# Performance work log

Measured on AMD Instinct MI355X. Metric: run time of the kernel, lower is better.

Reference implementation:

```python
import jax, jax.numpy as jnp
from jax import lax
import numpy as np

B, T, I, H, O = 2048, 512, 3, 128, 2


def _uniform(key, shape, scale):
    return jax.random.uniform(key, shape, jnp.float32, -scale, scale)


def setup_inputs() -> dict:
    key = jax.random.key(0)
    ks = jax.random.split(key, 12)
    s = 1.0 / np.sqrt(H)  # PyTorch LSTM init scale
    inp = {
        "x": jax.random.normal(ks[0], (B, T, I), jnp.float32),
        # layer 0: input size I
        "w_ih0": _uniform(ks[1], (4 * H, I), s),
        "w_hh0": _uniform(ks[2], (4 * H, H), s),
        "b_ih0": _uniform(ks[3], (4 * H,), s),
        "b_hh0": _uniform(ks[4], (4 * H,), s),
        # layer 1: input size H
        "w_ih1": _uniform(ks[5], (4 * H, H), s),
        "w_hh1": _uniform(ks[6], (4 * H, H), s),
        "b_ih1": _uniform(ks[7], (4 * H,), s),
        "b_hh1": _uniform(ks[8], (4 * H,), s),
        # final projection
        "fc_w": _uniform(ks[9], (O, H), 1.0 / np.sqrt(H)),
        "fc_b": _uniform(ks[10], (O,), 1.0 / np.sqrt(H)),
    }
    return inp


def _lstm_layer(x, w_ih, w_hh, b_ih, b_hh):
    # x: [B, T, D_in] -> hidden sequence [B, T, H]
    b, t, _ = x.shape
    h_dim = w_hh.shape[1]
    # precompute input projections for all timesteps (one big GEMM)
    x_proj = jnp.einsum("btd,gd->btg", x, w_ih) + b_ih + b_hh  # [B, T, 4H]
    x_proj = jnp.swapaxes(x_proj, 0, 1)  # [T, B, 4H]

    def step(carry, xt):
        h, c = carry
        gates = xt + h @ w_hh.T  # [B, 4H]
        i, f, g, o = jnp.split(gates, 4, axis=-1)  # PyTorch gate order i,f,g,o
        i = jax.nn.sigmoid(i)
        f = jax.nn.sigmoid(f)
        g = jnp.tanh(g)
        o = jax.nn.sigmoid(o)
        c = f * c + i * g
        h = o * jnp.tanh(c)
        return (h, c), h

    h0 = jnp.zeros((b, h_dim), x.dtype)
    c0 = jnp.zeros((b, h_dim), x.dtype)
    _, hs = lax.scan(step, (h0, c0), x_proj)  # hs: [T, B, H]
    return jnp.swapaxes(hs, 0, 1)  # [B, T, H]


def reference(x, w_ih0, w_hh0, b_ih0, b_hh0, w_ih1, w_hh1, b_ih1, b_hh1, fc_w, fc_b):
    h1 = _lstm_layer(x, w_ih0, w_hh0, b_ih0, b_hh0)   # [B, T, H]
    h2 = _lstm_layer(h1, w_ih1, w_hh1, b_ih1, b_hh1)  # [B, T, H]
    last = h2[:, -1, :]                                # [B, H]
    return last @ fc_w.T + fc_b                        # [B, O]
```

## Files before the change

kernel.cpp:

```cpp
#include <hip/hip_runtime.h>

#define B_   2048
#define T_   512
#define H_   128
#define G_   512
#define R_   8
#define NTHR 512

typedef _Float16 f16;
typedef _Float16 f16x8 __attribute__((ext_vector_type(8)));
typedef float    f32x4 __attribute__((ext_vector_type(4)));
typedef int      i32x2 __attribute__((ext_vector_type(2)));

#define OFF_W1    0
#define OFF_RING  131072
#define OFF_HB    139264
#define OFF_XT    143360
#define LDS_BYTES 145408

__device__ __forceinline__ float rcp_(float v) {
#if __has_builtin(__builtin_amdgcn_rcpf)
  return __builtin_amdgcn_rcpf(v);
#else
  return 1.0f / v;
#endif
}
__device__ __forceinline__ float sig_(float v)  { return rcp_(1.0f + __expf(-v)); }
__device__ __forceinline__ float tanh_(float v) { return 1.0f - 2.0f * rcp_(__expf(2.0f * v) + 1.0f); }

__device__ __forceinline__ f16x8 cvt8(const float* __restrict__ p) {
  float4 a = ((const float4*)p)[0];
  float4 b = ((const float4*)p)[1];
  f16x8 v;
  v[0]=(f16)a.x; v[1]=(f16)a.y; v[2]=(f16)a.z; v[3]=(f16)a.w;
  v[4]=(f16)b.x; v[5]=(f16)b.y; v[6]=(f16)b.z; v[7]=(f16)b.w;
  return v;
}
__device__ __forceinline__ f32x4 mfma16(f16x8 a, f16x8 b, f32x4 c) {
  return __builtin_amdgcn_mfma_f32_16x16x32_f16(a, b, c, 0, 0, 0);
}

__device__ __forceinline__ void pls2_(float a, float b, float& x, float& y) {
#if __has_builtin(__builtin_amdgcn_permlane32_swap)
  i32x2 r = __builtin_amdgcn_permlane32_swap(__float_as_int(a), __float_as_int(b),
                                             false, false);
  x = __int_as_float(r.x); y = __int_as_float(r.y);
#else
  asm volatile("v_permlane32_swap_b32 %0, %1" : "+v"(a), "+v"(b));
  x = a; y = b;
#endif
}

__global__ __launch_bounds__(NTHR, 2)
void lstm_v6(const float* __restrict__ x,
             const float* __restrict__ w_ih0, const float* __restrict__ w_hh0,
             const float* __restrict__ b_ih0, const float* __restrict__ b_hh0,
             const float* __restrict__ w_ih1, const float* __restrict__ w_hh1,
             const float* __restrict__ b_ih1, const float* __restrict__ b_hh1,
             const float* __restrict__ fc_w,  const float* __restrict__ fc_b,
             float* __restrict__ out)
{
  extern __shared__ char lds[];
  char*  w1L   = lds + OFF_W1;
  char*  ringB = lds + OFF_RING;
  char*  hBB   = lds + OFF_HB;
  char*  xT    = lds + OFF_XT;

  const int tid  = (int)threadIdx.x;
  const int lane = tid & 63;
  const int wv   = tid >> 6;
  const int n    = lane & 15;
  const int hi   = lane >> 4;
  const int u0   = wv * 16;
  const int blk  = (int)blockIdx.x;
  const int rsw  = (n & 7) << 4;

  for (int idx = tid; idx < G_*16; idx += NTHR) {
    const int g = idx >> 4, s7 = idx & 15;
    f16x8 v = cvt8(w_ih1 + g*H_ + s7*8);
    *(f16x8*)(w1L + g*256 + ((s7*16) ^ ((g&7)<<4))) = v;
  }
  for (int i = tid; i < 3584; i += NTHR) ((unsigned*)ringB)[i] = 0u;
  __syncthreads();

  float xr0 = 0.f, xr1 = 0.f, xr2 = 0.f;
  if (wv == 7) {
    const int tok = lane >> 3, r = lane & 7;
    const size_t base = (size_t)(blk*R_ + r) * T_;
    const float a0 = x[(base + tok)*3+0];
    const float a1 = x[(base + tok)*3+1];
    const float a2 = x[(base + tok)*3+2];
    f16* w = (f16*)(xT + tok*128 + r*16);
    w[0] = (f16)a0; w[1] = (f16)a1; w[2] = (f16)a2;
    xr0 = x[(base + 8 + tok)*3+0];
    xr1 = x[(base + 8 + tok)*3+1];
    xr2 = x[(base + 8 + tok)*3+2];
  }

  f16x8 whh0f[4][4], whh1f[4][4];
  #pragma unroll
  for (int q = 0; q < 4; ++q)
    #pragma unroll
    for (int kc = 0; kc < 4; ++kc) {
      const int off = (q*H_ + u0 + n)*H_ + kc*32 + hi*8;
      whh0f[q][kc] = cvt8(w_hh0 + off);
      whh1f[q][kc] = cvt8(w_hh1 + off);
    }
  f16x8 w0p[4];
  float b0[4], bP[4];
  #pragma unroll
  for (int q = 0; q < 4; ++q) {
    const int g = q*H_ + u0 + n;
    b0[q] = b_ih0[g] + b_hh0[g];
    bP[q] = b_ih1[g] + b_hh1[g];
    f16x8 z;
    #pragma unroll
    for (int e = 0; e < 8; ++e) z[e] = (f16)0.f;
    if (hi == 0) {
      z[0] = (f16)w_ih0[g*3+0];
      z[1] = (f16)w_ih0[g*3+1];
      z[2] = (f16)w_ih0[g*3+2];
    }
    w0p[q] = z;
  }

  int offA[4];
  #pragma unroll
  for (int kc = 0; kc < 4; ++kc)
    offA[kc] = (n&7)*256 + ((kc*64 + hi*16) ^ rsw);

  float cA0 = 0.f, cA1 = 0.f, cB0 = 0.f, cB1 = 0.f;
  f32x4 xpP[4];
  const int rowbase = (hi & 1)*4 + ((lane >= 32) ? 2 : 0);
  const int colb    = 2*(u0 + n);
  __syncthreads();

  for (int s = 0; s < T_ + 2; ++s) {
    if (wv == 7 && (s & 7) == 3) {
      const int c = s >> 3;
      const int tok = lane >> 3, r = lane & 7;
      if (c <= 61) {
        const size_t base = (size_t)(blk*R_ + r) * T_ + (8*(c+2) + tok);
        const float a0 = x[base*3+0], a1 = x[base*3+1], a2 = x[base*3+2];
        f16* w = (f16*)(xT + ((c+1)&1)*1024 + tok*128 + r*16);
        w[0] = (f16)xr0; w[1] = (f16)xr1; w[2] = (f16)xr2;
        xr0 = a0; xr1 = a1; xr2 = a2;
      } else if (c == 62) {
        f16* w = (f16*)(xT + ((c+1)&1)*1024 + tok*128 + r*16);
        w[0] = (f16)xr0; w[1] = (f16)xr1; w[2] = (f16)xr2;
      }
    }

    if ((s & 1) == 0 && s >= 2 && s <= T_) {
      const char* pa = ringB + ((n < 8) ? (((s-2)&3)*2048) : (((s-1)&3)*2048));
      #pragma unroll
      for (int q = 0; q < 4; ++q)
        { xpP[q][0]=bP[q]; xpP[q][1]=bP[q]; xpP[q][2]=bP[q]; xpP[q][3]=bP[q]; }
      #pragma unroll
      for (int kc = 0; kc < 4; ++kc) {
        const f16x8 a = *(const f16x8*)(pa + offA[kc]);
        #pragma unroll
        for (int q = 0; q < 4; ++q) {
          const f16x8 bf = *(const f16x8*)(w1L + (q*H_ + u0 + n)*256
                                           + ((kc*64 + hi*16) ^ rsw));
          xpP[q] = mfma16(a, bf, xpP[q]);
        }
      }
    }

    if (s < T_) {
      const f16x8 ax = *(const f16x8*)(xT + ((s>>3)&1)*1024 + (s&7)*128 + (n&7)*16);
      f32x4 acc[4];
      #pragma unroll
      for (int q = 0; q < 4; ++q) {
        f32x4 a; a[0]=b0[q]; a[1]=b0[q]; a[2]=b0[q]; a[3]=b0[q];
        acc[q] = mfma16(ax, w0p[q], a);
      }
      const char* pa = ringB + ((s-1)&3)*2048;
      #pragma unroll
      for (int kc = 0; kc < 4; ++kc) {
        const f16x8 af = *(const f16x8*)(pa + offA[kc]);
        #pragma unroll
        for (int q = 0; q < 4; ++q) acc[q] = mfma16(af, whh0f[q][kc], acc[q]);
      }
      char* wr = ringB + (s&3)*2048;
      float gA[4], gB[4], d0, d1;
      #pragma unroll
      for (int q = 0; q < 4; ++q) {
        pls2_(acc[q][0], acc[q][2], gA[q], d0);
        pls2_(acc[q][1], acc[q][3], gB[q], d1);
      }
      {
        const float iv = sig_(gA[0]), fv = sig_(gA[1]), gv = tanh_(gA[2]), ov = sig_(gA[3]);
        cA0 = fv*cA0 + iv*gv;
        const float h = ov * tanh_(cA0);
        *(f16*)(wr + rowbase*256 + (colb ^ (rowbase<<4))) = (f16)h;
      }
      {
        const float iv = sig_(gB[0]), fv = sig_(gB[1]), gv = tanh_(gB[2]), ov = sig_(gB[3]);
        cA1 = fv*cA1 + iv*gv;
        const float h = ov * tanh_(cA1);
        *(f16*)(wr + (rowbase+1)*256 + (colb ^ ((rowbase+1)<<4))) = (f16)h;
      }
    }

    if (s >= 2) {
      const bool odd = (s & 1);
      const char* pb = hBB + (s&1)*2048;
      f32x4 acc[4];
      #pragma unroll
      for (int q = 0; q < 4; ++q) acc[q] = xpP[q];
      #pragma unroll
      for (int kc = 0; kc < 4; ++kc) {
        const f16x8 af = *(const f16x8*)(pb + offA[kc]);
        #pragma unroll
        for (int q = 0; q < 4; ++q) acc[q] = mfma16(af, whh1f[q][kc], acc[q]);
      }
      char* wr = hBB + ((s+1)&1)*2048;
      float gA[4], gB[4];
      #pragma unroll
      for (int q = 0; q < 4; ++q) {
        float ex, ey, fx, fy;
        pls2_(acc[q][0], acc[q][2], ex, ey);
        gA[q] = odd ? ey : ex;
        pls2_(acc[q][1], acc[q][3], fx, fy);
        gB[q] = odd ? fy : fx;
      }
      {
        const float iv = sig_(gA[0]), fv = sig_(gA[1]), gv = tanh_(gA[2]), ov = sig_(gA[3]);
        cB0 = fv*cB0 + iv*gv;
        const float h = ov * tanh_(cB0);
        *(f16*)(wr + rowbase*256 + (colb ^ (rowbase<<4))) = (f16)h;
      }
      {
        const float iv = sig_(gB[0]), fv = sig_(gB[1]), gv = tanh_(gB[2]), ov = sig_(gB[3]);
        cB1 = fv*cB1 + iv*gv;
        const float h = ov * tanh_(cB1);
        *(f16*)(wr + (rowbase+1)*256 + (colb ^ ((rowbase+1)<<4))) = (f16)h;
      }
    }
    __syncthreads();
  }

  if (tid < R_*2) {
    const int r = tid >> 1, o = tid & 1;
    float acc = fc_b[o];
    #pragma unroll 4
    for (int d = 0; d < H_; ++d) {
      const f16 hv = *(const f16*)(hBB + r*256 + ((2*d) ^ ((r&7)<<4)));
      acc += (float)hv * fc_w[o*H_ + d];
    }
    out[(blk*R_ + r)*2 + o] = acc;
  }
}

extern "C" void kernel_launch(void* const* d_in, const int* in_sizes, int n_in,
                              void* d_out, int out_size, void* d_ws, size_t ws_size,
                              hipStream_t stream) {
  const float* x     = (const float*)d_in[0];
  const float* w_ih0 = (const float*)d_in[1];
  const float* w_hh0 = (const float*)d_in[2];
  const float* b_ih0 = (const float*)d_in[3];
  const float* b_hh0 = (const float*)d_in[4];
  const float* w_ih1 = (const float*)d_in[5];
  const float* w_hh1 = (const float*)d_in[6];
  const float* b_ih1 = (const float*)d_in[7];
  const float* b_hh1 = (const float*)d_in[8];
  const float* fc_w  = (const float*)d_in[9];
  const float* fc_b  = (const float*)d_in[10];
  (void)in_sizes; (void)n_in; (void)out_size; (void)d_ws; (void)ws_size;

  hipFuncSetAttribute((const void*)lstm_v6,
                      hipFuncAttributeMaxDynamicSharedMemorySize, LDS_BYTES);

  lstm_v6<<<B_/R_, NTHR, LDS_BYTES, stream>>>(
      x, w_ih0, w_hh0, b_ih0, b_hh0, w_ih1, w_hh1, b_ih1, b_hh1,
      fc_w, fc_b, (float*)d_out);
}
```

Before: 884.8 us.

## Batch layer-1 input projection over four timesteps and pack h stores in pairs

Enlarges the layer-0 hidden-state ring from 4 to 8 slots so the layer-1 input projection runs every fourth step over two timestep pairs, reusing each loaded W_ih1 fragment for two MFMAs. This halves the LDS weight reads for that projection. Separately, hidden-state writes are packed two f16 values per 32-bit store by exchanging with the neighbouring lane via DPP, so only even lanes write. The cost is a layer-1 pipeline two steps deeper, more LDS, and more accumulator registers, which may pressure the two-blocks-per-CU occupancy.

```diff
diff --git a/kernel.cpp b/kernel.cpp
--- a/kernel.cpp
+++ b/kernel.cpp
@@ -14,9 +14,9 @@
 
 #define OFF_W1    0
 #define OFF_RING  131072
-#define OFF_HB    139264
-#define OFF_XT    143360
-#define LDS_BYTES 145408
+#define OFF_HB    147456
+#define OFF_XT    151552
+#define LDS_BYTES 153600
 
 __device__ __forceinline__ float rcp_(float v) {
 #if __has_builtin(__builtin_amdgcn_rcpf)
@@ -51,8 +51,19 @@
 #endif
 }
 
+__device__ __forceinline__ unsigned packpair_(float h) {
+  const f16 hf = (f16)h;
+  unsigned u = (unsigned)__builtin_bit_cast(unsigned short, hf);
+#if __has_builtin(__builtin_amdgcn_mov_dpp)
+  unsigned p = (unsigned)__builtin_amdgcn_mov_dpp((int)u, 0xB1, 0xF, 0xF, true);
+#else
+  unsigned p = (unsigned)__shfl_xor((int)u, 1);
+#endif
+  return u | (p << 16);
+}
+
 __global__ __launch_bounds__(NTHR, 2)
-void lstm_v6(const float* __restrict__ x,
+void lstm_v8(const float* __restrict__ x,
              const float* __restrict__ w_ih0, const float* __restrict__ w_hh0,
              const float* __restrict__ b_ih0, const float* __restrict__ b_hh0,
              const float* __restrict__ w_ih1, const float* __restrict__ w_hh1,
@@ -80,7 +91,7 @@
     f16x8 v = cvt8(w_ih1 + g*H_ + s7*8);
     *(f16x8*)(w1L + g*256 + ((s7*16) ^ ((g&7)<<4))) = v;
   }
-  for (int i = tid; i < 3584; i += NTHR) ((unsigned*)ringB)[i] = 0u;
+  for (int i = tid; i < 5632; i += NTHR) ((unsigned*)ringB)[i] = 0u;
   __syncthreads();
 
   float xr0 = 0.f, xr1 = 0.f, xr2 = 0.f;
@@ -128,14 +139,19 @@
   #pragma unroll
   for (int kc = 0; kc < 4; ++kc)
     offA[kc] = (n&7)*256 + ((kc*64 + hi*16) ^ rsw);
+  int offB[4];
+  #pragma unroll
+  for (int kc = 0; kc < 4; ++kc)
+    offB[kc] = (kc*64 + hi*16) ^ rsw;
 
   float cA0 = 0.f, cA1 = 0.f, cB0 = 0.f, cB1 = 0.f;
-  f32x4 xpP[4];
+  f32x4 xpA[4], xpB[4];
   const int rowbase = (hi & 1)*4 + ((lane >= 32) ? 2 : 0);
-  const int colb    = 2*(u0 + n);
+  const int colb    = 2*(u0 + (n & ~1));
+  const bool wlane  = ((n & 1) == 0);
   __syncthreads();
 
-  for (int s = 0; s < T_ + 2; ++s) {
+  for (int s = 0; s < T_ + 4; ++s) {
     if (wv == 7 && (s & 7) == 3) {
       const int c = s >> 3;
       const int tok = lane >> 3, r = lane & 7;
@@ -151,19 +167,23 @@
       }
     }
 
-    if ((s & 1) == 0 && s >= 2 && s <= T_) {
-      const char* pa = ringB + ((n < 8) ? (((s-2)&3)*2048) : (((s-1)&3)*2048));
-      #pragma unroll
-      for (int q = 0; q < 4; ++q)
-        { xpP[q][0]=bP[q]; xpP[q][1]=bP[q]; xpP[q][2]=bP[q]; xpP[q][3]=bP[q]; }
+    if ((s & 3) == 0 && s >= 4 && s <= T_) {
+      const char* pa0 = ringB + ((n < 8) ? (((s-4)&7)*2048) : (((s-3)&7)*2048));
+      const char* pa1 = ringB + ((n < 8) ? (((s-2)&7)*2048) : (((s-1)&7)*2048));
+      #pragma unroll
+      for (int q = 0; q < 4; ++q) {
+        xpA[q][0]=bP[q]; xpA[q][1]=bP[q]; xpA[q][2]=bP[q]; xpA[q][3]=bP[q];
+        xpB[q][0]=bP[q]; xpB[q][1]=bP[q]; xpB[q][2]=bP[q]; xpB[q][3]=bP[q];
+      }
       #pragma unroll
       for (int kc = 0; kc < 4; ++kc) {
-        const f16x8 a = *(const f16x8*)(pa + offA[kc]);
+        const f16x8 a0 = *(const f16x8*)(pa0 + offA[kc]);
+        const f16x8 a1 = *(const f16x8*)(pa1 + offA[kc]);
         #pragma unroll
         for (int q = 0; q < 4; ++q) {
-          const f16x8 bf = *(const f16x8*)(w1L + (q*H_ + u0 + n)*256
-                                           + ((kc*64 + hi*16) ^ rsw));
-          xpP[q] = mfma16(a, bf, xpP[q]);
+          const f16x8 bf = *(const f16x8*)(w1L + (q*H_ + u0 + n)*256 + offB[kc]);
+          xpA[q] = mfma16(a0, bf, xpA[q]);
+          xpB[q] = mfma16(a1, bf, xpB[q]);
         }
       }
     }
@@ -176,14 +196,14 @@
         f32x4 a; a[0]=b0[q]; a[1]=b0[q]; a[2]=b0[q]; a[3]=b0[q];
         acc[q] = mfma16(ax, w0p[q], a);
       }
-      const char* pa = ringB + ((s-1)&3)*2048;
+      const char* pa = ringB + (((s-1)&7)*2048);
       #pragma unroll
       for (int kc = 0; kc < 4; ++kc) {
         const f16x8 af = *(const f16x8*)(pa + offA[kc]);
         #pragma unroll
         for (int q = 0; q < 4; ++q) acc[q] = mfma16(af, whh0f[q][kc], acc[q]);
       }
-      char* wr = ringB + (s&3)*2048;
+      char* wr = ringB + ((s&7)*2048);
       float gA[4], gB[4], d0, d1;
       #pragma unroll
       for (int q = 0; q < 4; ++q) {
@@ -193,50 +213,60 @@
       {
         const float iv = sig_(gA[0]), fv = sig_(gA[1]), gv = tanh_(gA[2]), ov = sig_(gA[3]);
         cA0 = fv*cA0 + iv*gv;
-        const float h = ov * tanh_(cA0);
-        *(f16*)(wr + rowbase*256 + (colb ^ (rowbase<<4))) = (f16)h;
+        const unsigned pk = packpair_(ov * tanh_(cA0));
+        if (wlane)
+          *(unsigned*)(wr + rowbase*256 + (colb ^ (rowbase<<4))) = pk;
       }
       {
         const float iv = sig_(gB[0]), fv = sig_(gB[1]), gv = tanh_(gB[2]), ov = sig_(gB[3]);
         cA1 = fv*cA1 + iv*gv;
-        const float h = ov * tanh_(cA1);
-        *(f16*)(wr + (rowbase+1)*256 + (colb ^ ((rowbase+1)<<4))) = (f16)h;
-      }
-    }
-
-    if (s >= 2) {
-      const bool odd = (s & 1);
+        const unsigned pk = packpair_(ov * tanh_(cA1));
+        if (wlane)
+          *(unsigned*)(wr + (rowbase+1)*256 + (colb ^ ((rowbase+1)<<4))) = pk;
+      }
+    }
+
+    if (s >= 4) {
+      const int  p   = s & 3;
+      const bool odd = (p & 1) != 0;
       const char* pb = hBB + (s&1)*2048;
       f32x4 acc[4];
-      #pragma unroll
-      for (int q = 0; q < 4; ++q) acc[q] = xpP[q];
+      if (p < 2) {
+        #pragma unroll
+        for (int q = 0; q < 4; ++q) acc[q] = xpA[q];
+      } else {
+        #pragma unroll
+        for (int q = 0; q < 4; ++q) acc[q] = xpB[q];
+      }
       #pragma unroll
       for (int kc = 0; kc < 4; ++kc) {
         const f16x8 af = *(const f16x8*)(pb + offA[kc]);
         #pragma unroll
         for (int q = 0; q < 4; ++q) acc[q] = mfma16(af, whh1f[q][kc], acc[q]);
       }
-      char* wr = hBB + ((s+1)&1)*2048;
+      char* wr = hBB + (((s+1)&1)*2048);
       float gA[4], gB[4];
       #pragma unroll
       for (int q = 0; q < 4; ++q) {
         float ex, ey, fx, fy;
         pls2_(acc[q][0], acc[q][2], ex, ey);
+        pls2_(acc[q][1], acc[q][3], fx, fy);
         gA[q] = odd ? ey : ex;
-        pls2_(acc[q][1], acc[q][3], fx, fy);
         gB[q] = odd ? fy : fx;
       }
       {
         const float iv = sig_(gA[0]), fv = sig_(gA[1]), gv = tanh_(gA[2]), ov = sig_(gA[3]);
         cB0 = fv*cB0 + iv*gv;
-        const float h = ov * tanh_(cB0);
-        *(f16*)(wr + rowbase*256 + (colb ^ (rowbase<<4))) = (f16)h;
+        const unsigned pk = packpair_(ov * tanh_(cB0));
+        if (wlane)
+          *(unsigned*)(wr + rowbase*256 + (colb ^ (rowbase<<4))) = pk;
       }
       {
         const float iv = sig_(gB[0]), fv = sig_(gB[1]), gv = tanh_(gB[2]), ov = sig_(gB[3]);
         cB1 = fv*cB1 + iv*gv;
-        const float h = ov * tanh_(cB1);
-        *(f16*)(wr + (rowbase+1)*256 + (colb ^ ((rowbase+1)<<4))) = (f16)h;
+        const unsigned pk = packpair_(ov * tanh_(cB1));
+        if (wlane)
+          *(unsigned*)(wr + (rowbase+1)*256 + (colb ^ ((rowbase+1)<<4))) = pk;
       }
     }
     __syncthreads();
@@ -270,10 +300,10 @@
   const float* fc_b  = (const float*)d_in[10];
   (void)in_sizes; (void)n_in; (void)out_size; (void)d_ws; (void)ws_size;
 
-  hipFuncSetAttribute((const void*)lstm_v6,
+  hipFuncSetAttribute((const void*)lstm_v8,
                       hipFuncAttributeMaxDynamicSharedMemorySize, LDS_BYTES);
 
-  lstm_v6<<<B_/R_, NTHR, LDS_BYTES, stream>>>(
+  lstm_v8<<<B_/R_, NTHR, LDS_BYTES, stream>>>(
       x, w_ih0, w_hh0, b_ih0, b_hh0, w_ih1, w_hh1, b_ih1, b_hh1,
       fc_w, fc_b, (float*)d_out);
 }
```

After: 1.183 ms. +33.8%, slower.
